# Optimization experiments

Measured on AMD Instinct MI355X. Metric: run time of the kernel, lower is better.

The kernel has to match this reference:

```python
import jax, jax.numpy as jnp
import numpy as np

H = 1024  # HIDDEN_LAYER_SIZE

def _xavier(key, shape, gain=0.01):
    fan_out, fan_in = shape
    a = gain * np.sqrt(6.0 / (fan_in + fan_out))
    return jax.random.uniform(key, shape, jnp.float32, -a, a)

def setup_inputs() -> dict:
    key = jax.random.key(0)
    ks = jax.random.split(key, 7)
    B = 65536
    white_features = jax.random.uniform(ks[0], (B, 768), jnp.float32)
    black_features = jax.random.uniform(ks[1], (B, 768), jnp.float32)
    stm = jax.random.uniform(ks[2], (B, 1), jnp.float32)
    return {
        "white_features": white_features,
        "black_features": black_features,
        "stm": stm,
        "ft_w": _xavier(ks[3], (H, 768)),
        "ft_b": jnp.zeros((H,), jnp.float32),
        "l1_w": _xavier(ks[4], (8, 2 * H)),
        "l1_b": jnp.zeros((8,), jnp.float32),
        "l2_w": _xavier(ks[5], (32, 8)),
        "l2_b": jnp.zeros((32,), jnp.float32),
        "l3_w": _xavier(ks[6], (1, 32)),
        "l3_b": jnp.zeros((1,), jnp.float32),
    }

def reference(white_features, black_features, stm, ft_w, ft_b,
              l1_w, l1_b, l2_w, l2_b, l3_w, l3_b):
    w = white_features @ ft_w.T + ft_b  # [B, H]
    b = black_features @ ft_w.T + ft_b  # [B, H]
    acc = stm * jnp.concatenate([w, b], axis=1) + (1.0 - stm) * jnp.concatenate([b, w], axis=1)
    l1_x = jnp.clip(acc, 0.0, 1.0)
    l2_x = jnp.clip(l1_x @ l1_w.T + l1_b, 0.0, 1.0)
    l3_x = jnp.clip(l2_x @ l2_w.T + l2_b, 0.0, 1.0)
    raw_output = l3_x @ l3_w.T + l3_b  # [B, 1]
    output = jax.nn.sigmoid(raw_output)
    return (output, raw_output)
```

## Files before the change

kernel.cpp:

```cpp
#include <hip/hip_runtime.h>
#include <cmath>

typedef float f4_t __attribute__((ext_vector_type(4)));
typedef long  l2_t __attribute__((ext_vector_type(2)));

#define B_TOTAL   65536
#define FTW_SCALE 1024.0f
#define INV_SCALE (1.0f/1024.0f)

__device__ __forceinline__ int pk8(float a, float b, float c, float d) {
    int v = __builtin_amdgcn_cvt_pk_fp8_f32(a, b, 0, false);
    return  __builtin_amdgcn_cvt_pk_fp8_f32(c, d, v, true);
}
__device__ __forceinline__ float clip01(float x) { return fminf(fmaxf(x, 0.f), 1.f); }

__global__ void pack_ftw_kernel(const float* __restrict__ ftw, char* __restrict__ ws)
{
    int t    = blockIdx.x * 256 + threadIdx.x;
    int lane = t & 63;
    int ncp  = (t >> 6) & 31;
    int kk   = t >> 11;
    int nl = lane & 15, q = (lane >> 4) & 3;
    int k0 = kk * 32 + q * 8;
    const float* p0 = ftw + (size_t)(ncp * 32 + nl) * 768 + k0;
    const float* p1 = p0 + 16 * 768;
    float4 x0 = *(const float4*)p0;
    float4 x1 = *(const float4*)(p0 + 4);
    float4 y0 = *(const float4*)p1;
    float4 y1 = *(const float4*)(p1 + 4);
    int4 o;
    o.x = pk8(x0.x*FTW_SCALE, x0.y*FTW_SCALE, x0.z*FTW_SCALE, x0.w*FTW_SCALE);
    o.y = pk8(x1.x*FTW_SCALE, x1.y*FTW_SCALE, x1.z*FTW_SCALE, x1.w*FTW_SCALE);
    o.z = pk8(y0.x*FTW_SCALE, y0.y*FTW_SCALE, y0.z*FTW_SCALE, y0.w*FTW_SCALE);
    o.w = pk8(y1.x*FTW_SCALE, y1.y*FTW_SCALE, y1.z*FTW_SCALE, y1.w*FTW_SCALE);
    *(int4*)(ws + (size_t)t * 16) = o;
}

__global__ __launch_bounds__(256, 3) void nnue_fused_kernel(
    const float* __restrict__ wf,  const float* __restrict__ bfeat,
    const float* __restrict__ stm, const char*  __restrict__ ftw8,
    const float* __restrict__ ftb, const float* __restrict__ l1w,
    const float* __restrict__ l1b, const float* __restrict__ l2w,
    const float* __restrict__ l2b, const float* __restrict__ l3w,
    const float* __restrict__ l3b, float* __restrict__ out)
{
    __shared__ char  Ald[24 * 2048];
    __shared__ float l1part[4][32][8];

    const int t    = threadIdx.x;
    const int lane = t & 63;
    const int wave = t >> 6;
    const int nl   = lane & 15;
    const int q    = (lane >> 4) & 3;
    const int s0   = blockIdx.x * 32;

    {
        const int kpar = t >> 7;
        const int tt   = t & 127;
        const int p    = tt >> 6;
        const int sl   = tt & 63;
        const int snl  = sl & 15, sq = (sl >> 4) & 3;
        const float* base = p ? bfeat : wf;
        const float* r0 = base + (size_t)(s0 + snl) * 768;
        const float* r1 = r0 + 16 * 768;
        char* dst = &Ald[p * 1024 + sl * 16];
        #pragma unroll 4
        for (int pass = 0; pass < 12; ++pass) {
            int kk = pass * 2 + kpar;
            int k0 = kk * 32 + sq * 8;
            float4 x0 = *(const float4*)(r0 + k0);
            float4 x1 = *(const float4*)(r0 + k0 + 4);
            float4 y0 = *(const float4*)(r1 + k0);
            float4 y1 = *(const float4*)(r1 + k0 + 4);
            int4 o;
            o.x = pk8(x0.x, x0.y, x0.z, x0.w);
            o.y = pk8(x1.x, x1.y, x1.z, x1.w);
            o.z = pk8(y0.x, y0.y, y0.z, y0.w);
            o.w = pk8(y1.x, y1.y, y1.z, y1.w);
            *(int4*)(dst + kk * 2048) = o;
        }
    }

    float s_lo[4], s_hi[4];
    #pragma unroll
    for (int r = 0; r < 4; ++r) {
        s_lo[r] = stm[s0 + q * 4 + r];
        s_hi[r] = stm[s0 + 16 + q * 4 + r];
    }

    __syncthreads();

    float pacc[2][4][8];
    #pragma unroll
    for (int mh = 0; mh < 2; ++mh)
        #pragma unroll
        for (int r = 0; r < 4; ++r)
            #pragma unroll
            for (int o = 0; o < 8; ++o) pacc[mh][r][o] = 0.f;

    const char* ap = &Ald[lane * 16];

    #pragma unroll 1
    for (int ng = 0; ng < 4; ++ng) {
        f4_t aW0[4], aW1[4], aB0[4], aB1[4];
        #pragma unroll
        for (int nb = 0; nb < 4; ++nb) {
            aW0[nb] = (f4_t){0.f,0.f,0.f,0.f};
            aW1[nb] = (f4_t){0.f,0.f,0.f,0.f};
            aB0[nb] = (f4_t){0.f,0.f,0.f,0.f};
            aB1[nb] = (f4_t){0.f,0.f,0.f,0.f};
        }
        const char* bp = ftw8 + (size_t)(wave * 8 + ng * 2) * 1024 + lane * 16;
        l2_t bc0 = *(const l2_t*)(bp);
        l2_t bc1 = *(const l2_t*)(bp + 1024);

        #pragma unroll 2
        for (int kk = 0; kk < 24; ++kk) {
            l2_t bn0, bn1;
            if (kk < 23) {
                bn0 = *(const l2_t*)(bp + (size_t)(kk + 1) * 32768);
                bn1 = *(const l2_t*)(bp + (size_t)(kk + 1) * 32768 + 1024);
            }
            l2_t aw = *(const l2_t*)(ap + kk * 2048);
            l2_t ab = *(const l2_t*)(ap + kk * 2048 + 1024);

            aW0[0] = __builtin_amdgcn_mfma_f32_16x16x32_fp8_fp8(aw.x, bc0.x, aW0[0], 0,0,0);
            aW1[0] = __builtin_amdgcn_mfma_f32_16x16x32_fp8_fp8(aw.y, bc0.x, aW1[0], 0,0,0);
            aB0[0] = __builtin_amdgcn_mfma_f32_16x16x32_fp8_fp8(ab.x, bc0.x, aB0[0], 0,0,0);
            aB1[0] = __builtin_amdgcn_mfma_f32_16x16x32_fp8_fp8(ab.y, bc0.x, aB1[0], 0,0,0);
            aW0[1] = __builtin_amdgcn_mfma_f32_16x16x32_fp8_fp8(aw.x, bc0.y, aW0[1], 0,0,0);
            aW1[1] = __builtin_amdgcn_mfma_f32_16x16x32_fp8_fp8(aw.y, bc0.y, aW1[1], 0,0,0);
            aB0[1] = __builtin_amdgcn_mfma_f32_16x16x32_fp8_fp8(ab.x, bc0.y, aB0[1], 0,0,0);
            aB1[1] = __builtin_amdgcn_mfma_f32_16x16x32_fp8_fp8(ab.y, bc0.y, aB1[1], 0,0,0);
            aW0[2] = __builtin_amdgcn_mfma_f32_16x16x32_fp8_fp8(aw.x, bc1.x, aW0[2], 0,0,0);
            aW1[2] = __builtin_amdgcn_mfma_f32_16x16x32_fp8_fp8(aw.y, bc1.x, aW1[2], 0,0,0);
            aB0[2] = __builtin_amdgcn_mfma_f32_16x16x32_fp8_fp8(ab.x, bc1.x, aB0[2], 0,0,0);
            aB1[2] = __builtin_amdgcn_mfma_f32_16x16x32_fp8_fp8(ab.y, bc1.x, aB1[2], 0,0,0);
            aW0[3] = __builtin_amdgcn_mfma_f32_16x16x32_fp8_fp8(aw.x, bc1.y, aW0[3], 0,0,0);
            aW1[3] = __builtin_amdgcn_mfma_f32_16x16x32_fp8_fp8(aw.y, bc1.y, aW1[3], 0,0,0);
            aB0[3] = __builtin_amdgcn_mfma_f32_16x16x32_fp8_fp8(ab.x, bc1.y, aB0[3], 0,0,0);
            aB1[3] = __builtin_amdgcn_mfma_f32_16x16x32_fp8_fp8(ab.y, bc1.y, aB1[3], 0,0,0);

            if (kk < 23) { bc0 = bn0; bc1 = bn1; }
        }

        #pragma unroll
        for (int nb = 0; nb < 4; ++nb) {
            int col = wave * 256 + ng * 64 + nb * 16 + nl;
            float bias = ftb[col];
            const float* l1c = l1w + col;
            float lo[8], hi[8];
            #pragma unroll
            for (int o = 0; o < 8; ++o) {
                lo[o] = l1c[o * 2048];
                hi[o] = l1c[o * 2048 + 1024];
            }
            #pragma unroll
            for (int r = 0; r < 4; ++r) {
                float w0 = fmaf(aW0[nb][r], INV_SCALE, bias);
                float b0 = fmaf(aB0[nb][r], INV_SCALE, bias);
                float w1 = fmaf(aW1[nb][r], INV_SCALE, bias);
                float b1 = fmaf(aB1[nb][r], INV_SCALE, bias);
                float d0 = w0 - b0, d1 = w1 - b1;
                float f0 = clip01(fmaf( s_lo[r], d0, b0));
                float g0 = clip01(fmaf(-s_lo[r], d0, w0));
                float f1 = clip01(fmaf( s_hi[r], d1, b1));
                float g1 = clip01(fmaf(-s_hi[r], d1, w1));
                #pragma unroll
                for (int o = 0; o < 8; ++o) {
                    pacc[0][r][o] = fmaf(f0, lo[o], fmaf(g0, hi[o], pacc[0][r][o]));
                    pacc[1][r][o] = fmaf(f1, lo[o], fmaf(g1, hi[o], pacc[1][r][o]));
                }
            }
        }
    }

    #pragma unroll
    for (int m = 1; m < 16; m <<= 1)
        #pragma unroll
        for (int mh = 0; mh < 2; ++mh)
            #pragma unroll
            for (int r = 0; r < 4; ++r)
                #pragma unroll
                for (int o = 0; o < 8; ++o)
                    pacc[mh][r][o] += __shfl_xor(pacc[mh][r][o], m);

    if (nl == 0) {
        #pragma unroll
        for (int mh = 0; mh < 2; ++mh)
            #pragma unroll
            for (int r = 0; r < 4; ++r)
                #pragma unroll
                for (int o = 0; o < 8; ++o)
                    l1part[wave][mh * 16 + q * 4 + r][o] = pacc[mh][r][o];
    }
    __syncthreads();

    if (t < 32) {
        float v[8];
        #pragma unroll
        for (int o = 0; o < 8; ++o)
            v[o] = clip01(l1part[0][t][o] + l1part[1][t][o] +
                          l1part[2][t][o] + l1part[3][t][o] + l1b[o]);
        float raw = l3b[0];
        #pragma unroll
        for (int u = 0; u < 32; ++u) {
            float h = l2b[u];
            #pragma unroll
            for (int o = 0; o < 8; ++o) h = fmaf(v[o], l2w[u * 8 + o], h);
            h = clip01(h);
            raw = fmaf(h, l3w[u], raw);
        }
        out[s0 + t]           = 1.0f / (1.0f + expf(-raw));
        out[B_TOTAL + s0 + t] = raw;
    }
}

extern "C" void kernel_launch(void* const* d_in, const int* in_sizes, int n_in,
                              void* d_out, int out_size, void* d_ws, size_t ws_size,
                              hipStream_t stream)
{
    const float* wf  = (const float*)d_in[0];
    const float* bf  = (const float*)d_in[1];
    const float* stm = (const float*)d_in[2];
    const float* ftw = (const float*)d_in[3];
    const float* ftb = (const float*)d_in[4];
    const float* l1w = (const float*)d_in[5];
    const float* l1b = (const float*)d_in[6];
    const float* l2w = (const float*)d_in[7];
    const float* l2b = (const float*)d_in[8];
    const float* l3w = (const float*)d_in[9];
    const float* l3b = (const float*)d_in[10];
    char* ws8 = (char*)d_ws;

    hipLaunchKernelGGL(pack_ftw_kernel, dim3(192), dim3(256), 0, stream, ftw, ws8);
    hipLaunchKernelGGL(nnue_fused_kernel, dim3(2048), dim3(256), 0, stream,
                       wf, bf, stm, ws8, ftb, l1w, l1b, l2w, l2b, l3w, l3b,
                       (float*)d_out);
}
```

Before: 636.5 us.

## Halve MFMA accumulator tile per group and vectorize L1 epilogue with packed float2

The feature-transform loop now processes 8 column groups of 32 instead of 4 groups of 64, so each wave keeps 8 MFMA accumulators instead of 16. The K loop is restructured to consume two K steps per iteration with the packed B layout, prefetching both. The L1 partial products are kept as float2 vectors so the compiler can emit packed FMA instructions. The aim is lower register pressure, and possibly higher occupancy, plus cheaper epilogue arithmetic. The cost is more B-fragment loads per A reuse and twice as many epilogue passes.

Result: faster. 597.4 us (-6.1%).

```diff
diff --git a/kernel.cpp b/kernel.cpp
--- a/kernel.cpp
+++ b/kernel.cpp
@@ -2,6 +2,7 @@
 #include <cmath>
 
 typedef float f4_t __attribute__((ext_vector_type(4)));
+typedef float f2_t __attribute__((ext_vector_type(2)));
 typedef long  l2_t __attribute__((ext_vector_type(2)));
 
 #define B_TOTAL   65536
@@ -90,86 +91,86 @@
 
     __syncthreads();
 
-    float pacc[2][4][8];
+    f2_t pacc[2][4][4];
     #pragma unroll
     for (int mh = 0; mh < 2; ++mh)
         #pragma unroll
         for (int r = 0; r < 4; ++r)
             #pragma unroll
-            for (int o = 0; o < 8; ++o) pacc[mh][r][o] = 0.f;
+            for (int i = 0; i < 4; ++i) pacc[mh][r][i] = (f2_t){0.f, 0.f};
 
     const char* ap = &Ald[lane * 16];
 
     #pragma unroll 1
-    for (int ng = 0; ng < 4; ++ng) {
-        f4_t aW0[4], aW1[4], aB0[4], aB1[4];
-        #pragma unroll
-        for (int nb = 0; nb < 4; ++nb) {
-            aW0[nb] = (f4_t){0.f,0.f,0.f,0.f};
-            aW1[nb] = (f4_t){0.f,0.f,0.f,0.f};
-            aB0[nb] = (f4_t){0.f,0.f,0.f,0.f};
-            aB1[nb] = (f4_t){0.f,0.f,0.f,0.f};
-        }
-        const char* bp = ftw8 + (size_t)(wave * 8 + ng * 2) * 1024 + lane * 16;
+    for (int ng = 0; ng < 8; ++ng) {
+        f4_t acc[4][2];
+        #pragma unroll
+        for (int m = 0; m < 4; ++m) {
+            acc[m][0] = (f4_t){0.f,0.f,0.f,0.f};
+            acc[m][1] = (f4_t){0.f,0.f,0.f,0.f};
+        }
+        const char* bp = ftw8 + (size_t)(wave * 8 + ng) * 1024 + (size_t)lane * 16;
         l2_t bc0 = *(const l2_t*)(bp);
-        l2_t bc1 = *(const l2_t*)(bp + 1024);
+        l2_t bc1 = *(const l2_t*)(bp + 32768);
 
         #pragma unroll 2
-        for (int kk = 0; kk < 24; ++kk) {
-            l2_t bn0, bn1;
-            if (kk < 23) {
-                bn0 = *(const l2_t*)(bp + (size_t)(kk + 1) * 32768);
-                bn1 = *(const l2_t*)(bp + (size_t)(kk + 1) * 32768 + 1024);
-            }
-            l2_t aw = *(const l2_t*)(ap + kk * 2048);
-            l2_t ab = *(const l2_t*)(ap + kk * 2048 + 1024);
-
-            aW0[0] = __builtin_amdgcn_mfma_f32_16x16x32_fp8_fp8(aw.x, bc0.x, aW0[0], 0,0,0);
-            aW1[0] = __builtin_amdgcn_mfma_f32_16x16x32_fp8_fp8(aw.y, bc0.x, aW1[0], 0,0,0);
-            aB0[0] = __builtin_amdgcn_mfma_f32_16x16x32_fp8_fp8(ab.x, bc0.x, aB0[0], 0,0,0);
-            aB1[0] = __builtin_amdgcn_mfma_f32_16x16x32_fp8_fp8(ab.y, bc0.x, aB1[0], 0,0,0);
-            aW0[1] = __builtin_amdgcn_mfma_f32_16x16x32_fp8_fp8(aw.x, bc0.y, aW0[1], 0,0,0);
-            aW1[1] = __builtin_amdgcn_mfma_f32_16x16x32_fp8_fp8(aw.y, bc0.y, aW1[1], 0,0,0);
-            aB0[1] = __builtin_amdgcn_mfma_f32_16x16x32_fp8_fp8(ab.x, bc0.y, aB0[1], 0,0,0);
-            aB1[1] = __builtin_amdgcn_mfma_f32_16x16x32_fp8_fp8(ab.y, bc0.y, aB1[1], 0,0,0);
-            aW0[2] = __builtin_amdgcn_mfma_f32_16x16x32_fp8_fp8(aw.x, bc1.x, aW0[2], 0,0,0);
-            aW1[2] = __builtin_amdgcn_mfma_f32_16x16x32_fp8_fp8(aw.y, bc1.x, aW1[2], 0,0,0);
-            aB0[2] = __builtin_amdgcn_mfma_f32_16x16x32_fp8_fp8(ab.x, bc1.x, aB0[2], 0,0,0);
-            aB1[2] = __builtin_amdgcn_mfma_f32_16x16x32_fp8_fp8(ab.y, bc1.x, aB1[2], 0,0,0);
-            aW0[3] = __builtin_amdgcn_mfma_f32_16x16x32_fp8_fp8(aw.x, bc1.y, aW0[3], 0,0,0);
-            aW1[3] = __builtin_amdgcn_mfma_f32_16x16x32_fp8_fp8(aw.y, bc1.y, aW1[3], 0,0,0);
-            aB0[3] = __builtin_amdgcn_mfma_f32_16x16x32_fp8_fp8(ab.x, bc1.y, aB0[3], 0,0,0);
-            aB1[3] = __builtin_amdgcn_mfma_f32_16x16x32_fp8_fp8(ab.y, bc1.y, aB1[3], 0,0,0);
-
-            if (kk < 23) { bc0 = bn0; bc1 = bn1; }
-        }
-
-        #pragma unroll
-        for (int nb = 0; nb < 4; ++nb) {
-            int col = wave * 256 + ng * 64 + nb * 16 + nl;
+        for (int kg = 0; kg < 12; ++kg) {
+            int pf0 = (kg < 11) ? (2 * kg + 2) : 22;
+            int pf1 = (kg < 11) ? (2 * kg + 3) : 23;
+            l2_t bn0 = *(const l2_t*)(bp + (size_t)pf0 * 32768);
+            l2_t bn1 = *(const l2_t*)(bp + (size_t)pf1 * 32768);
+
+            l2_t aw = *(const l2_t*)(ap + (2 * kg) * 2048);
+            l2_t ab = *(const l2_t*)(ap + (2 * kg) * 2048 + 1024);
+            acc[0][0] = __builtin_amdgcn_mfma_f32_16x16x32_fp8_fp8(aw.x, bc0.x, acc[0][0], 0,0,0);
+            acc[1][0] = __builtin_amdgcn_mfma_f32_16x16x32_fp8_fp8(aw.y, bc0.x, acc[1][0], 0,0,0);
+            acc[2][0] = __builtin_amdgcn_mfma_f32_16x16x32_fp8_fp8(ab.x, bc0.x, acc[2][0], 0,0,0);
+            acc[3][0] = __builtin_amdgcn_mfma_f32_16x16x32_fp8_fp8(ab.y, bc0.x, acc[3][0], 0,0,0);
+            acc[0][1] = __builtin_amdgcn_mfma_f32_16x16x32_fp8_fp8(aw.x, bc0.y, acc[0][1], 0,0,0);
+            acc[1][1] = __builtin_amdgcn_mfma_f32_16x16x32_fp8_fp8(aw.y, bc0.y, acc[1][1], 0,0,0);
+            acc[2][1] = __builtin_amdgcn_mfma_f32_16x16x32_fp8_fp8(ab.x, bc0.y, acc[2][1], 0,0,0);
+            acc[3][1] = __builtin_amdgcn_mfma_f32_16x16x32_fp8_fp8(ab.y, bc0.y, acc[3][1], 0,0,0);
+
+            l2_t aw2 = *(const l2_t*)(ap + (2 * kg + 1) * 2048);
+            l2_t ab2 = *(const l2_t*)(ap + (2 * kg + 1) * 2048 + 1024);
+            acc[0][0] = __builtin_amdgcn_mfma_f32_16x16x32_fp8_fp8(aw2.x, bc1.x, acc[0][0], 0,0,0);
+            acc[1][0] = __builtin_amdgcn_mfma_f32_16x16x32_fp8_fp8(aw2.y, bc1.x, acc[1][0], 0,0,0);
+            acc[2][0] = __builtin_amdgcn_mfma_f32_16x16x32_fp8_fp8(ab2.x, bc1.x, acc[2][0], 0,0,0);
+            acc[3][0] = __builtin_amdgcn_mfma_f32_16x16x32_fp8_fp8(ab2.y, bc1.x, acc[3][0], 0,0,0);
+            acc[0][1] = __builtin_amdgcn_mfma_f32_16x16x32_fp8_fp8(aw2.x, bc1.y, acc[0][1], 0,0,0);
+            acc[1][1] = __builtin_amdgcn_mfma_f32_16x16x32_fp8_fp8(aw2.y, bc1.y, acc[1][1], 0,0,0);
+            acc[2][1] = __builtin_amdgcn_mfma_f32_16x16x32_fp8_fp8(ab2.x, bc1.y, acc[2][1], 0,0,0);
+            acc[3][1] = __builtin_amdgcn_mfma_f32_16x16x32_fp8_fp8(ab2.y, bc1.y, acc[3][1], 0,0,0);
+
+            bc0 = bn0; bc1 = bn1;
+        }
+
+        #pragma unroll
+        for (int nb = 0; nb < 2; ++nb) {
+            int col = wave * 256 + ng * 32 + nb * 16 + nl;
             float bias = ftb[col];
             const float* l1c = l1w + col;
-            float lo[8], hi[8];
-            #pragma unroll
-            for (int o = 0; o < 8; ++o) {
-                lo[o] = l1c[o * 2048];
-                hi[o] = l1c[o * 2048 + 1024];
+            f2_t lo2[4], hi2[4];
+            #pragma unroll
+            for (int i = 0; i < 4; ++i) {
+                lo2[i] = (f2_t){l1c[(2*i) * 2048],        l1c[(2*i+1) * 2048]};
+                hi2[i] = (f2_t){l1c[(2*i) * 2048 + 1024], l1c[(2*i+1) * 2048 + 1024]};
             }
             #pragma unroll
             for (int r = 0; r < 4; ++r) {
-                float w0 = fmaf(aW0[nb][r], INV_SCALE, bias);
-                float b0 = fmaf(aB0[nb][r], INV_SCALE, bias);
-                float w1 = fmaf(aW1[nb][r], INV_SCALE, bias);
-                float b1 = fmaf(aB1[nb][r], INV_SCALE, bias);
+                float w0 = fmaf(acc[0][nb][r], INV_SCALE, bias);
+                float w1 = fmaf(acc[1][nb][r], INV_SCALE, bias);
+                float b0 = fmaf(acc[2][nb][r], INV_SCALE, bias);
+                float b1 = fmaf(acc[3][nb][r], INV_SCALE, bias);
                 float d0 = w0 - b0, d1 = w1 - b1;
                 float f0 = clip01(fmaf( s_lo[r], d0, b0));
                 float g0 = clip01(fmaf(-s_lo[r], d0, w0));
                 float f1 = clip01(fmaf( s_hi[r], d1, b1));
                 float g1 = clip01(fmaf(-s_hi[r], d1, w1));
                 #pragma unroll
-                for (int o = 0; o < 8; ++o) {
-                    pacc[0][r][o] = fmaf(f0, lo[o], fmaf(g0, hi[o], pacc[0][r][o]));
-                    pacc[1][r][o] = fmaf(f1, lo[o], fmaf(g1, hi[o], pacc[1][r][o]));
+                for (int i = 0; i < 4; ++i) {
+                    pacc[0][r][i] += f0 * lo2[i] + g0 * hi2[i];
+                    pacc[1][r][i] += f1 * lo2[i] + g1 * hi2[i];
                 }
             }
         }
@@ -182,8 +183,10 @@
             #pragma unroll
             for (int r = 0; r < 4; ++r)
                 #pragma unroll
-                for (int o = 0; o < 8; ++o)
-                    pacc[mh][r][o] += __shfl_xor(pacc[mh][r][o], m);
+                for (int i = 0; i < 4; ++i) {
+                    pacc[mh][r][i].x += __shfl_xor(pacc[mh][r][i].x, m);
+                    pacc[mh][r][i].y += __shfl_xor(pacc[mh][r][i].y, m);
+                }
 
     if (nl == 0) {
         #pragma unroll
@@ -191,8 +194,10 @@
             #pragma unroll
             for (int r = 0; r < 4; ++r)
                 #pragma unroll
-                for (int o = 0; o < 8; ++o)
-                    l1part[wave][mh * 16 + q * 4 + r][o] = pacc[mh][r][o];
+                for (int i = 0; i < 4; ++i) {
+                    l1part[wave][mh * 16 + q * 4 + r][2*i]   = pacc[mh][r][i].x;
+                    l1part[wave][mh * 16 + q * 4 + r][2*i+1] = pacc[mh][r][i].y;
+                }
     }
     __syncthreads();
 
```
